# Kernel optimization log

Measured on AMD Instinct MI355X. Metric: run time of the kernel, lower is better.

Reference implementation:

```python
import jax, jax.numpy as jnp
import numpy as np

B, D, R, E, L = 8192, 2048, 64, 4, 3


def setup_inputs() -> dict:
    key = jax.random.key(0)
    ks = jax.random.split(key, 6)
    inputs = jax.random.normal(ks[0], (B, D), dtype=jnp.float32)
    # xavier-normal-ish init for low-rank factors
    U = jax.random.normal(ks[1], (L, E, D, R), dtype=jnp.float32) * (2.0 / (D + R)) ** 0.5
    V = jax.random.normal(ks[2], (L, E, D, R), dtype=jnp.float32) * (2.0 / (D + R)) ** 0.5
    C = jax.random.normal(ks[3], (L, E, R, R), dtype=jnp.float32) * (1.0 / R) ** 0.5
    gate_w = jax.random.normal(ks[4], (E, D), dtype=jnp.float32) * (1.0 / D) ** 0.5
    bias = jnp.zeros((L, D), dtype=jnp.float32)
    return {"inputs": inputs, "U": U, "V": V, "C": C, "gate_w": gate_w, "bias": bias}


def reference(inputs, U, V, C, gate_w, bias):
    x0 = inputs                      # (B, D)
    x_l = inputs
    for i in range(L):
        # gating scores per expert, softmax over experts
        gs = jax.nn.softmax(x_l @ gate_w.T, axis=-1)            # (B, E)
        # low-rank cross: tanh(V^T x) -> tanh(C .) -> U .
        vx = jnp.tanh(jnp.einsum('edr,bd->ber', V[i], x_l))     # (B, E, R)
        cx = jnp.tanh(jnp.einsum('esr,ber->bes', C[i], vx))     # (B, E, R)
        uv = jnp.einsum('eds,bes->bed', U[i], cx)               # (B, E, D)
        dot = (uv + bias[i][None, None, :]) * x0[:, None, :]    # (B, E, D)
        x_l = jnp.einsum('bed,be->bd', dot, gs) + x_l           # MoE combine + residual
    return x_l
```

## Files before the change

kernel.cpp:

```cpp
#include <hip/hip_runtime.h>
#include <cmath>

#define Bb 8192
#define Dd 2048
#define Rr 64
#define Ee 4
#define Ll 3

typedef __bf16 bf16x8 __attribute__((ext_vector_type(8)));
typedef float f32x4 __attribute__((ext_vector_type(4)));
typedef unsigned short u16x8 __attribute__((ext_vector_type(8)));
typedef unsigned short u16x4 __attribute__((ext_vector_type(4)));

__device__ __forceinline__ unsigned short f2bf(float f){
  unsigned u = __builtin_bit_cast(unsigned, f);
  u += 0x7fffu + ((u >> 16) & 1u);
  return (unsigned short)(u >> 16);
}
__device__ __forceinline__ float bf2f(unsigned short h){
  return __builtin_bit_cast(float, ((unsigned)h) << 16);
}

__global__ __launch_bounds__(256) void prep_w_k(const float* __restrict__ U,
                                                const float* __restrict__ V,
                                                const float* __restrict__ C,
                                                const float* __restrict__ gw,
                                                unsigned short* __restrict__ VfT,
                                                unsigned short* __restrict__ UfT,
                                                unsigned short* __restrict__ cb16,
                                                unsigned short* __restrict__ gw16){
  const int NV = Ll * 256 * Dd;
  const int NU = Ll * Dd * 256;
  const int NC = Ll * Ee * Rr * Rr;
  const int NG = Ee * Dd;
  const int total = NV + NU + NC + NG;
  for (int idx = blockIdx.x * blockDim.x + threadIdx.x; idx < total; idx += gridDim.x * blockDim.x){
    if (idx < NV){
      int l = idx / (256 * Dd); int rem = idx - l * 256 * Dd;
      int n = rem / Dd, d = rem - n * Dd;
      int e = n >> 6, r = n & 63;
      VfT[idx] = f2bf(V[(((size_t)l * Ee + e) * Dd + d) * Rr + r]);
    } else if (idx < NV + NU){
      int j = idx - NV;
      int l = j / (Dd * 256); int rem = j - l * Dd * 256;
      int d = rem / 256, k = rem - d * 256;
      int e = k >> 6, s = k & 63;
      UfT[j] = f2bf(U[(((size_t)l * Ee + e) * Dd + d) * Rr + s]);
    } else if (idx < NV + NU + NC){
      int j = idx - NV - NU;
      cb16[j] = f2bf(C[j]);
    } else {
      int j = idx - NV - NU - NC;
      gw16[j] = f2bf(gw[j]);
    }
  }
}

template<bool AF32>
__global__ __launch_bounds__(256) void gate_k(const void* __restrict__ xv,
                                              const unsigned short* __restrict__ gw16,
                                              float* __restrict__ gs){
  const int lane = threadIdx.x & 63;
  const int w = threadIdx.x >> 6;
  const int row = blockIdx.x * 4 + w;
  float s0 = 0.f, s1 = 0.f, s2 = 0.f, s3 = 0.f;
  #pragma unroll
  for (int c = 0; c < 4; c++){
    const int k = c * 512 + lane * 8;
    float xf[8];
    if constexpr (AF32){
      const float* xr = (const float*)xv + (size_t)row * Dd + k;
      f32x4 v0 = *(const f32x4*)xr;
      f32x4 v1 = *(const f32x4*)(xr + 4);
      #pragma unroll
      for (int u = 0; u < 4; u++){ xf[u] = v0[u]; xf[4 + u] = v1[u]; }
    } else {
      u16x8 xvv = *(const u16x8*)((const unsigned short*)xv + (size_t)row * Dd + k);
      #pragma unroll
      for (int u = 0; u < 8; u++) xf[u] = bf2f(xvv[u]);
    }
    u16x8 g0v = *(const u16x8*)(gw16 + 0 * Dd + k);
    u16x8 g1v = *(const u16x8*)(gw16 + 1 * Dd + k);
    u16x8 g2v = *(const u16x8*)(gw16 + 2 * Dd + k);
    u16x8 g3v = *(const u16x8*)(gw16 + 3 * Dd + k);
    #pragma unroll
    for (int u = 0; u < 8; u++){
      s0 += xf[u] * bf2f(g0v[u]);
      s1 += xf[u] * bf2f(g1v[u]);
      s2 += xf[u] * bf2f(g2v[u]);
      s3 += xf[u] * bf2f(g3v[u]);
    }
  }
  #pragma unroll
  for (int m = 1; m < 64; m <<= 1){
    s0 += __shfl_xor(s0, m, 64);
    s1 += __shfl_xor(s1, m, 64);
    s2 += __shfl_xor(s2, m, 64);
    s3 += __shfl_xor(s3, m, 64);
  }
  if (lane == 0){
    float mx = fmaxf(fmaxf(s0, s1), fmaxf(s2, s3));
    float e0 = __expf(s0 - mx), e1 = __expf(s1 - mx), e2 = __expf(s2 - mx), e3 = __expf(s3 - mx);
    float inv = 1.f / (e0 + e1 + e2 + e3);
    f32x4 g; g[0] = e0 * inv; g[1] = e1 * inv; g[2] = e2 * inv; g[3] = e3 * inv;
    *(f32x4*)(gs + (size_t)row * 4) = g;
  }
}

template<bool AF32>
__global__ __launch_bounds__(256) void gemm1_k(const void* __restrict__ Av,
                                               const unsigned short* __restrict__ BT,
                                               float* __restrict__ vxp){
  const int bm0 = blockIdx.x * 64;
  const int bn0 = blockIdx.y * 128;
  const int z   = blockIdx.z;
  const int kc0 = z * 512;
  const int tid = threadIdx.x;
  const int lane = tid & 63;
  const int wv = tid >> 6;
  const int wm = wv >> 1, wn = wv & 1;

  __shared__ __align__(16) char smraw[27648];
  unsigned short (*As)[72] = (unsigned short (*)[72])smraw;
  unsigned short (*Bs)[72] = (unsigned short (*)[72])(smraw + 9216);
  float (*epi)[132] = (float (*)[132])smraw;

  f32x4 acc[2][4] = {};
  const int arow = tid >> 2;
  const int aseg = tid & 3;

  const float* Af = (const float*)Av;
  const unsigned short* Ab = (const unsigned short*)Av;

  f32x4 a4[4]; u16x8 ar[2]; u16x8 br[4];
  if constexpr (AF32){
    #pragma unroll
    for (int j = 0; j < 4; j++)
      a4[j] = *(const f32x4*)(Af + (size_t)(bm0 + arow) * Dd + kc0 + aseg * 16 + j * 4);
  } else {
    ar[0] = *(const u16x8*)(Ab + (size_t)(bm0 + arow) * Dd + kc0 + aseg * 16);
    ar[1] = *(const u16x8*)(Ab + (size_t)(bm0 + arow) * Dd + kc0 + aseg * 16 + 8);
  }
  br[0] = *(const u16x8*)(BT + (size_t)(bn0 + arow) * Dd + kc0 + aseg * 16);
  br[1] = *(const u16x8*)(BT + (size_t)(bn0 + arow) * Dd + kc0 + aseg * 16 + 8);
  br[2] = *(const u16x8*)(BT + (size_t)(bn0 + arow + 64) * Dd + kc0 + aseg * 16);
  br[3] = *(const u16x8*)(BT + (size_t)(bn0 + arow + 64) * Dd + kc0 + aseg * 16 + 8);

  for (int k0 = kc0; k0 < kc0 + 512; k0 += 64){
    __syncthreads();
    if constexpr (AF32){
      u16x8 av0, av1;
      #pragma unroll
      for (int j = 0; j < 4; j++){
        av0[j] = f2bf(a4[0][j]); av0[4 + j] = f2bf(a4[1][j]);
        av1[j] = f2bf(a4[2][j]); av1[4 + j] = f2bf(a4[3][j]);
      }
      *(u16x8*)(&As[arow][aseg * 16])     = av0;
      *(u16x8*)(&As[arow][aseg * 16 + 8]) = av1;
    } else {
      *(u16x8*)(&As[arow][aseg * 16])     = ar[0];
      *(u16x8*)(&As[arow][aseg * 16 + 8]) = ar[1];
    }
    *(u16x8*)(&Bs[arow][aseg * 16])          = br[0];
    *(u16x8*)(&Bs[arow][aseg * 16 + 8])      = br[1];
    *(u16x8*)(&Bs[arow + 64][aseg * 16])     = br[2];
    *(u16x8*)(&Bs[arow + 64][aseg * 16 + 8]) = br[3];
    __syncthreads();

    int kn = k0 + 64;
    if (kn < kc0 + 512){
      if constexpr (AF32){
        #pragma unroll
        for (int j = 0; j < 4; j++)
          a4[j] = *(const f32x4*)(Af + (size_t)(bm0 + arow) * Dd + kn + aseg * 16 + j * 4);
      } else {
        ar[0] = *(const u16x8*)(Ab + (size_t)(bm0 + arow) * Dd + kn + aseg * 16);
        ar[1] = *(const u16x8*)(Ab + (size_t)(bm0 + arow) * Dd + kn + aseg * 16 + 8);
      }
      br[0] = *(const u16x8*)(BT + (size_t)(bn0 + arow) * Dd + kn + aseg * 16);
      br[1] = *(const u16x8*)(BT + (size_t)(bn0 + arow) * Dd + kn + aseg * 16 + 8);
      br[2] = *(const u16x8*)(BT + (size_t)(bn0 + arow + 64) * Dd + kn + aseg * 16);
      br[3] = *(const u16x8*)(BT + (size_t)(bn0 + arow + 64) * Dd + kn + aseg * 16 + 8);
    }

    #pragma unroll
    for (int ks = 0; ks < 2; ks++){
      bf16x8 af[2];
      #pragma unroll
      for (int mi = 0; mi < 2; mi++)
        af[mi] = *reinterpret_cast<const bf16x8*>(&As[wm * 32 + mi * 16 + (lane & 15)][ks * 32 + (lane >> 4) * 8]);
      #pragma unroll
      for (int nj = 0; nj < 4; nj++){
        bf16x8 bfr = *reinterpret_cast<const bf16x8*>(&Bs[wn * 64 + nj * 16 + (lane & 15)][ks * 32 + (lane >> 4) * 8]);
        #pragma unroll
        for (int mi = 0; mi < 2; mi++)
          acc[mi][nj] = __builtin_amdgcn_mfma_f32_16x16x32_bf16(af[mi], bfr, acc[mi][nj], 0, 0, 0);
      }
    }
  }

  float* outz = vxp + (size_t)z * Bb * 256;
  #pragma unroll
  for (int h = 0; h < 2; h++){
    __syncthreads();
    if (wm == h){
      #pragma unroll
      for (int mi = 0; mi < 2; mi++)
        #pragma unroll
        for (int nj = 0; nj < 4; nj++)
          #pragma unroll
          for (int q = 0; q < 4; q++)
            epi[mi * 16 + (lane >> 4) * 4 + q][wn * 64 + nj * 16 + (lane & 15)] = acc[mi][nj][q];
    }
    __syncthreads();
    #pragma unroll
    for (int c = 0; c < 4; c++){
      int idx = c * 256 + tid;
      int r = idx >> 5;
      int col = (idx & 31) * 4;
      *(f32x4*)(outz + (size_t)(bm0 + h * 32 + r) * 256 + bn0 + col) = *(const f32x4*)&epi[r][col];
    }
  }
}

__global__ __launch_bounds__(256) void gemm2_k(const float* __restrict__ vxp,
                                               const unsigned short* __restrict__ cb,
                                               const float* __restrict__ gs,
                                               unsigned short* __restrict__ wb){
  const int bm0 = blockIdx.x * 64;
  const int e   = blockIdx.y;
  const int tid = threadIdx.x;
  const int lane = tid & 63;
  const int wv = tid >> 6;
  const int wm = wv >> 1, wn = wv & 1;

  __shared__ __align__(16) char smraw[18432];
  unsigned short (*As)[72] = (unsigned short (*)[72])smraw;
  unsigned short (*Bs)[72] = (unsigned short (*)[72])(smraw + 9216);
  unsigned short (*epi)[72] = (unsigned short (*)[72])smraw;

  const int arow = tid >> 2;
  const int aseg = tid & 3;

  f32x4 t[4];
  #pragma unroll
  for (int j = 0; j < 4; j++)
    t[j] = *(const f32x4*)(vxp + (size_t)(bm0 + arow) * 256 + e * 64 + aseg * 16 + j * 4);
  #pragma unroll
  for (int z = 1; z < 4; z++)
    #pragma unroll
    for (int j = 0; j < 4; j++)
      t[j] += *(const f32x4*)(vxp + (size_t)z * Bb * 256 + (size_t)(bm0 + arow) * 256 + e * 64 + aseg * 16 + j * 4);
  u16x8 av0, av1;
  #pragma unroll
  for (int j = 0; j < 4; j++){
    av0[j] = f2bf(tanhf(t[0][j])); av0[4 + j] = f2bf(tanhf(t[1][j]));
    av1[j] = f2bf(tanhf(t[2][j])); av1[4 + j] = f2bf(tanhf(t[3][j]));
  }
  *(u16x8*)(&As[arow][aseg * 16]) = av0;
  *(u16x8*)(&As[arow][aseg * 16 + 8]) = av1;
  *(u16x8*)(&Bs[arow][aseg * 16])     = *(const u16x8*)(cb + e * 4096 + arow * 64 + aseg * 16);
  *(u16x8*)(&Bs[arow][aseg * 16 + 8]) = *(const u16x8*)(cb + e * 4096 + arow * 64 + aseg * 16 + 8);
  __syncthreads();

  f32x4 acc[2][2] = {};
  #pragma unroll
  for (int kk = 0; kk < 2; kk++){
    bf16x8 af[2];
    #pragma unroll
    for (int mi = 0; mi < 2; mi++)
      af[mi] = *reinterpret_cast<const bf16x8*>(&As[wm * 32 + mi * 16 + (lane & 15)][kk * 32 + (lane >> 4) * 8]);
    #pragma unroll
    for (int nj = 0; nj < 2; nj++){
      bf16x8 bfr = *reinterpret_cast<const bf16x8*>(&Bs[wn * 32 + nj * 16 + (lane & 15)][kk * 32 + (lane >> 4) * 8]);
      #pragma unroll
      for (int mi = 0; mi < 2; mi++)
        acc[mi][nj] = __builtin_amdgcn_mfma_f32_16x16x32_bf16(af[mi], bfr, acc[mi][nj], 0, 0, 0);
    }
  }

  __syncthreads();
  #pragma unroll
  for (int mi = 0; mi < 2; mi++)
    #pragma unroll
    for (int nj = 0; nj < 2; nj++)
      #pragma unroll
      for (int q = 0; q < 4; q++){
        int row = wm * 32 + mi * 16 + (lane >> 4) * 4 + q;
        int col = wn * 32 + nj * 16 + (lane & 15);
        float g = gs[(size_t)(bm0 + row) * 4 + e];
        epi[row][col] = f2bf(g * tanhf(acc[mi][nj][q]));
      }
  __syncthreads();
  #pragma unroll
  for (int c = 0; c < 2; c++){
    int idx = c * 256 + tid;
    int row = idx >> 3;
    int col = (idx & 7) * 8;
    *(u16x8*)(wb + (size_t)(bm0 + row) * 256 + e * 64 + col) = *(const u16x8*)(&epi[row][col]);
  }
}

template<int MODE>
__global__ __launch_bounds__(256, 4) void gemm3_k(const unsigned short* __restrict__ A,
                                                  const unsigned short* __restrict__ BT,
                                                  const float* __restrict__ x0f,
                                                  unsigned short* __restrict__ xst,
                                                  const float* __restrict__ biasrow,
                                                  float* __restrict__ out){
  const int bm0 = blockIdx.x * 64;
  const int bn0 = blockIdx.y * 128;
  const int tid = threadIdx.x;
  const int lane = tid & 63;
  const int wv = tid >> 6;
  const int wm = wv >> 1, wn = wv & 1;

  __shared__ __align__(16) char smraw[17408];
  unsigned short (*As)[40] = (unsigned short (*)[40])smraw;
  unsigned short (*Bs)[40] = (unsigned short (*)[40])(smraw + 5120);
  float (*epi)[132] = (float (*)[132])smraw;

  f32x4 acc[2][4] = {};
  const int arow = tid >> 2;
  const int aseg = tid & 3;

  f32x4 x0p[8];
  u16x4 xsp[8];
  #pragma unroll
  for (int h = 0; h < 2; h++)
    #pragma unroll
    for (int c = 0; c < 4; c++){
      int idx = c * 256 + tid;
      int r = idx >> 5;
      int col = (idx & 31) * 4;
      size_t o = (size_t)(bm0 + h * 32 + r) * Dd + bn0 + col;
      x0p[h * 4 + c] = *(const f32x4*)(x0f + o);
      if constexpr (MODE != 0) xsp[h * 4 + c] = *(const u16x4*)(xst + o);
    }

  u16x8 areg  = *(const u16x8*)(A  + (size_t)(bm0 + arow) * 256 + aseg * 8);
  u16x8 breg0 = *(const u16x8*)(BT + (size_t)(bn0 + arow) * 256 + aseg * 8);
  u16x8 breg1 = *(const u16x8*)(BT + (size_t)(bn0 + arow + 64) * 256 + aseg * 8);

  for (int k0 = 0; k0 < 256; k0 += 32){
    __syncthreads();
    *(u16x8*)(&As[arow][aseg * 8]) = areg;
    *(u16x8*)(&Bs[arow][aseg * 8]) = breg0;
    *(u16x8*)(&Bs[arow + 64][aseg * 8]) = breg1;
    __syncthreads();
    if (k0 + 32 < 256){
      areg  = *(const u16x8*)(A  + (size_t)(bm0 + arow) * 256 + k0 + 32 + aseg * 8);
      breg0 = *(const u16x8*)(BT + (size_t)(bn0 + arow) * 256 + k0 + 32 + aseg * 8);
      breg1 = *(const u16x8*)(BT + (size_t)(bn0 + arow + 64) * 256 + k0 + 32 + aseg * 8);
    }
    bf16x8 af[2];
    #pragma unroll
    for (int mi = 0; mi < 2; mi++)
      af[mi] = *reinterpret_cast<const bf16x8*>(&As[wm * 32 + mi * 16 + (lane & 15)][(lane >> 4) * 8]);
    #pragma unroll
    for (int nj = 0; nj < 4; nj++){
      bf16x8 bfr = *reinterpret_cast<const bf16x8*>(&Bs[wn * 64 + nj * 16 + (lane & 15)][(lane >> 4) * 8]);
      #pragma unroll
      for (int mi = 0; mi < 2; mi++)
        acc[mi][nj] = __builtin_amdgcn_mfma_f32_16x16x32_bf16(af[mi], bfr, acc[mi][nj], 0, 0, 0);
    }
  }

  #pragma unroll
  for (int h = 0; h < 2; h++){
    __syncthreads();
    if (wm == h){
      #pragma unroll
      for (int mi = 0; mi < 2; mi++)
        #pragma unroll
        for (int nj = 0; nj < 4; nj++)
          #pragma unroll
          for (int q = 0; q < 4; q++)
            epi[mi * 16 + (lane >> 4) * 4 + q][wn * 64 + nj * 16 + (lane & 15)] = acc[mi][nj][q];
    }
    __syncthreads();
    #pragma unroll
    for (int c = 0; c < 4; c++){
      int idx = c * 256 + tid;
      int r = idx >> 5;
      int col = (idx & 31) * 4;
      int row = bm0 + h * 32 + r;
      size_t o = (size_t)row * Dd + bn0 + col;
      f32x4 y = *(const f32x4*)&epi[r][col];
      f32x4 x0v = x0p[h * 4 + c];
      f32x4 bv  = *(const f32x4*)(biasrow + bn0 + col);
      f32x4 xo;
      if constexpr (MODE == 0){
        xo = x0v;
      } else {
        u16x4 xv = xsp[h * 4 + c];
        #pragma unroll
        for (int j = 0; j < 4; j++) xo[j] = bf2f(xv[j]);
      }
      f32x4 xn;
      #pragma unroll
      for (int j = 0; j < 4; j++) xn[j] = xo[j] + x0v[j] * (bv[j] + y[j]);
      if constexpr (MODE == 2){
        *(f32x4*)(out + o) = xn;
      } else {
        u16x4 xnb;
        #pragma unroll
        for (int j = 0; j < 4; j++) xnb[j] = f2bf(xn[j]);
        *(u16x4*)(xst + o) = xnb;
      }
    }
  }
}

extern "C" void kernel_launch(void* const* d_in, const int* in_sizes, int n_in,
                              void* d_out, int out_size, void* d_ws, size_t ws_size,
                              hipStream_t stream){
  (void)in_sizes; (void)n_in; (void)out_size;
  const float* inp  = (const float*)d_in[0];
  const float* U    = (const float*)d_in[1];
  const float* V    = (const float*)d_in[2];
  const float* C    = (const float*)d_in[3];
  const float* gw   = (const float*)d_in[4];
  const float* bias = (const float*)d_in[5];
  float* out = (float*)d_out;

  char* ws = (char*)d_ws;
  size_t o = 0;
  unsigned short* xb  = (unsigned short*)(ws + o); o += (size_t)Bb * Dd * 2;
  float*          vxp = (float*)(ws + o);          o += (size_t)4 * Bb * 256 * 4;
  unsigned short* wb  = (unsigned short*)(ws + o); o += (size_t)Bb * 256 * 2;
  float*          gsb = (float*)(ws + o);          o += (size_t)Bb * 4 * 4;
  unsigned short* vft = (unsigned short*)(ws + o); o += (size_t)Ll * 256 * Dd * 2;
  unsigned short* uft = (unsigned short*)(ws + o); o += (size_t)Ll * Dd * 256 * 2;
  unsigned short* cb16= (unsigned short*)(ws + o); o += (size_t)Ll * Ee * Rr * Rr * 2;
  unsigned short* g16 = (unsigned short*)(ws + o); o += (size_t)Ee * Dd * 2;
  if (ws_size < o) return;

  prep_w_k<<<1024, 256, 0, stream>>>(U, V, C, gw, vft, uft, cb16, g16);

  for (int l = 0; l < Ll; l++){
    if (l == 0){
      gate_k<true><<<Bb / 4, 256, 0, stream>>>(inp, g16, gsb);
      gemm1_k<true><<<dim3(Bb / 64, 2, 4), 256, 0, stream>>>(inp, vft + (size_t)l * 256 * Dd, vxp);
    } else {
      gate_k<false><<<Bb / 4, 256, 0, stream>>>(xb, g16, gsb);
      gemm1_k<false><<<dim3(Bb / 64, 2, 4), 256, 0, stream>>>(xb, vft + (size_t)l * 256 * Dd, vxp);
    }
    gemm2_k<<<dim3(Bb / 64, Ee), 256, 0, stream>>>(vxp, cb16 + (size_t)l * Ee * Rr * Rr, gsb, wb);
    const unsigned short* uftl = uft + (size_t)l * Dd * 256;
    if (l == 0)
      gemm3_k<0><<<dim3(Bb / 64, Dd / 128), 256, 0, stream>>>(wb, uftl, inp, xb, bias + (size_t)l * Dd, out);
    else if (l == 1)
      gemm3_k<1><<<dim3(Bb / 64, Dd / 128), 256, 0, stream>>>(wb, uftl, inp, xb, bias + (size_t)l * Dd, out);
    else
      gemm3_k<2><<<dim3(Bb / 64, Dd / 128), 256, 0, stream>>>(wb, uftl, inp, xb, bias + (size_t)l * Dd, out);
  }
}
```

Measured before the change: 248.2 us.

## Fuse gating logits into gemm3 epilogue, store split-K partials and x0 as bf16

Gate logits for the next layer are now computed in the gemm3 epilogue as per-column-tile partial dot products and reduced with softmax inside gemm2. This removes the separate gate kernel, which re-read the full activation matrix for layers 1 and 2. The split-K partials from gemm1 are stored as bf16 instead of fp32, halving that round trip. A bf16 copy of the input is made once and used as x0 in every gemm3 epilogue, and the x0 and x_l prefetch before the main loop is dropped. The costs are extra bf16 rounding of the partial sums and x0, plus an extra cast kernel.

Result: faster. 218.0 us (-12.2%).

```diff
diff --git a/kernel.cpp b/kernel.cpp
--- a/kernel.cpp
+++ b/kernel.cpp
@@ -19,6 +19,17 @@
 }
 __device__ __forceinline__ float bf2f(unsigned short h){
   return __builtin_bit_cast(float, ((unsigned)h) << 16);
+}
+
+__global__ __launch_bounds__(256) void cast_x_k(const float* __restrict__ x,
+                                                unsigned short* __restrict__ xb0){
+  const int n4 = Bb * Dd / 4;
+  for (int i = blockIdx.x * blockDim.x + threadIdx.x; i < n4; i += gridDim.x * blockDim.x){
+    f32x4 v = *((const f32x4*)x + i);
+    u16x4 o;
+    o[0] = f2bf(v[0]); o[1] = f2bf(v[1]); o[2] = f2bf(v[2]); o[3] = f2bf(v[3]);
+    *((u16x4*)xb0 + i) = o;
+  }
 }
 
 __global__ __launch_bounds__(256) void prep_w_k(const float* __restrict__ U,
@@ -110,7 +121,7 @@
 template<bool AF32>
 __global__ __launch_bounds__(256) void gemm1_k(const void* __restrict__ Av,
                                                const unsigned short* __restrict__ BT,
-                                               float* __restrict__ vxp){
+                                               unsigned short* __restrict__ vxp){
   const int bm0 = blockIdx.x * 64;
   const int bn0 = blockIdx.y * 128;
   const int z   = blockIdx.z;
@@ -199,7 +210,7 @@
     }
   }
 
-  float* outz = vxp + (size_t)z * Bb * 256;
+  unsigned short* outz = vxp + (size_t)z * Bb * 256;
   #pragma unroll
   for (int h = 0; h < 2; h++){
     __syncthreads();
@@ -218,14 +229,20 @@
       int idx = c * 256 + tid;
       int r = idx >> 5;
       int col = (idx & 31) * 4;
-      *(f32x4*)(outz + (size_t)(bm0 + h * 32 + r) * 256 + bn0 + col) = *(const f32x4*)&epi[r][col];
-    }
-  }
-}
-
-__global__ __launch_bounds__(256) void gemm2_k(const float* __restrict__ vxp,
+      f32x4 v = *(const f32x4*)&epi[r][col];
+      u16x4 ov;
+      #pragma unroll
+      for (int j = 0; j < 4; j++) ov[j] = f2bf(v[j]);
+      *(u16x4*)(outz + (size_t)(bm0 + h * 32 + r) * 256 + bn0 + col) = ov;
+    }
+  }
+}
+
+template<bool FROMPLOG>
+__global__ __launch_bounds__(256) void gemm2_k(const unsigned short* __restrict__ vxp,
                                                const unsigned short* __restrict__ cb,
-                                               const float* __restrict__ gs,
+                                               const float* __restrict__ gsb,
+                                               const float* __restrict__ plog,
                                                unsigned short* __restrict__ wb){
   const int bm0 = blockIdx.x * 64;
   const int e   = blockIdx.y;
@@ -234,28 +251,53 @@
   const int wv = tid >> 6;
   const int wm = wv >> 1, wn = wv & 1;
 
-  __shared__ __align__(16) char smraw[18432];
+  __shared__ __align__(16) char smraw[19456];
   unsigned short (*As)[72] = (unsigned short (*)[72])smraw;
   unsigned short (*Bs)[72] = (unsigned short (*)[72])(smraw + 9216);
+  float (*gs_l)[4] = (float (*)[4])(smraw + 18432);
   unsigned short (*epi)[72] = (unsigned short (*)[72])smraw;
+
+  if constexpr (FROMPLOG){
+    int r = tid >> 2, q = tid & 3;
+    f32x4 s = {0.f, 0.f, 0.f, 0.f};
+    #pragma unroll
+    for (int ci = 0; ci < 4; ci++)
+      s += *(const f32x4*)(plog + ((size_t)(q * 4 + ci) * Bb + bm0 + r) * 4);
+    #pragma unroll
+    for (int j = 0; j < 4; j++){
+      s[j] += __shfl_xor(s[j], 1, 64);
+      s[j] += __shfl_xor(s[j], 2, 64);
+    }
+    if (q == 0){
+      float mx = fmaxf(fmaxf(s[0], s[1]), fmaxf(s[2], s[3]));
+      float e0 = __expf(s[0] - mx), e1 = __expf(s[1] - mx), e2 = __expf(s[2] - mx), e3 = __expf(s[3] - mx);
+      float inv = 1.f / (e0 + e1 + e2 + e3);
+      f32x4 g; g[0] = e0 * inv; g[1] = e1 * inv; g[2] = e2 * inv; g[3] = e3 * inv;
+      *(f32x4*)&gs_l[r][0] = g;
+    }
+  } else {
+    if (tid < 64) *(f32x4*)&gs_l[tid][0] = *(const f32x4*)(gsb + (size_t)(bm0 + tid) * 4);
+  }
 
   const int arow = tid >> 2;
   const int aseg = tid & 3;
 
-  f32x4 t[4];
-  #pragma unroll
-  for (int j = 0; j < 4; j++)
-    t[j] = *(const f32x4*)(vxp + (size_t)(bm0 + arow) * 256 + e * 64 + aseg * 16 + j * 4);
-  #pragma unroll
-  for (int z = 1; z < 4; z++)
-    #pragma unroll
-    for (int j = 0; j < 4; j++)
-      t[j] += *(const f32x4*)(vxp + (size_t)z * Bb * 256 + (size_t)(bm0 + arow) * 256 + e * 64 + aseg * 16 + j * 4);
+  float tv[16];
+  #pragma unroll
+  for (int j = 0; j < 16; j++) tv[j] = 0.f;
+  #pragma unroll
+  for (int z = 0; z < 4; z++){
+    const unsigned short* vz = vxp + ((size_t)z * Bb + bm0 + arow) * 256 + e * 64 + aseg * 16;
+    u16x8 p0 = *(const u16x8*)vz;
+    u16x8 p1 = *(const u16x8*)(vz + 8);
+    #pragma unroll
+    for (int j = 0; j < 8; j++){ tv[j] += bf2f(p0[j]); tv[8 + j] += bf2f(p1[j]); }
+  }
   u16x8 av0, av1;
   #pragma unroll
   for (int j = 0; j < 4; j++){
-    av0[j] = f2bf(tanhf(t[0][j])); av0[4 + j] = f2bf(tanhf(t[1][j]));
-    av1[j] = f2bf(tanhf(t[2][j])); av1[4 + j] = f2bf(tanhf(t[3][j]));
+    av0[j] = f2bf(tanhf(tv[j]));     av0[4 + j] = f2bf(tanhf(tv[4 + j]));
+    av1[j] = f2bf(tanhf(tv[8 + j])); av1[4 + j] = f2bf(tanhf(tv[12 + j]));
   }
   *(u16x8*)(&As[arow][aseg * 16]) = av0;
   *(u16x8*)(&As[arow][aseg * 16 + 8]) = av1;
@@ -288,7 +330,7 @@
       for (int q = 0; q < 4; q++){
         int row = wm * 32 + mi * 16 + (lane >> 4) * 4 + q;
         int col = wn * 32 + nj * 16 + (lane & 15);
-        float g = gs[(size_t)(bm0 + row) * 4 + e];
+        float g = gs_l[row][e];
         epi[row][col] = f2bf(g * tanhf(acc[mi][nj][q]));
       }
   __syncthreads();
@@ -301,13 +343,16 @@
   }
 }
 
-template<int MODE>
+template<int MODE, bool X0BF>
 __global__ __launch_bounds__(256, 4) void gemm3_k(const unsigned short* __restrict__ A,
                                                   const unsigned short* __restrict__ BT,
                                                   const float* __restrict__ x0f,
+                                                  const unsigned short* __restrict__ x0b,
                                                   unsigned short* __restrict__ xst,
                                                   const float* __restrict__ biasrow,
-                                                  float* __restrict__ out){
+                                                  float* __restrict__ out,
+                                                  const unsigned short* __restrict__ gw16,
+                                                  float* __restrict__ plog){
   const int bm0 = blockIdx.x * 64;
   const int bn0 = blockIdx.y * 128;
   const int tid = threadIdx.x;
@@ -323,20 +368,6 @@
   f32x4 acc[2][4] = {};
   const int arow = tid >> 2;
   const int aseg = tid & 3;
-
-  f32x4 x0p[8];
-  u16x4 xsp[8];
-  #pragma unroll
-  for (int h = 0; h < 2; h++)
-    #pragma unroll
-    for (int c = 0; c < 4; c++){
-      int idx = c * 256 + tid;
-      int r = idx >> 5;
-      int col = (idx & 31) * 4;
-      size_t o = (size_t)(bm0 + h * 32 + r) * Dd + bn0 + col;
-      x0p[h * 4 + c] = *(const f32x4*)(x0f + o);
-      if constexpr (MODE != 0) xsp[h * 4 + c] = *(const u16x4*)(xst + o);
-    }
 
   u16x8 areg  = *(const u16x8*)(A  + (size_t)(bm0 + arow) * 256 + aseg * 8);
   u16x8 breg0 = *(const u16x8*)(BT + (size_t)(bn0 + arow) * 256 + aseg * 8);
@@ -387,13 +418,20 @@
       int row = bm0 + h * 32 + r;
       size_t o = (size_t)row * Dd + bn0 + col;
       f32x4 y = *(const f32x4*)&epi[r][col];
-      f32x4 x0v = x0p[h * 4 + c];
-      f32x4 bv  = *(const f32x4*)(biasrow + bn0 + col);
+      f32x4 bv = *(const f32x4*)(biasrow + bn0 + col);
+      f32x4 x0v;
+      if constexpr (X0BF){
+        u16x4 xv = *(const u16x4*)(x0b + o);
+        #pragma unroll
+        for (int j = 0; j < 4; j++) x0v[j] = bf2f(xv[j]);
+      } else {
+        x0v = *(const f32x4*)(x0f + o);
+      }
       f32x4 xo;
       if constexpr (MODE == 0){
         xo = x0v;
       } else {
-        u16x4 xv = xsp[h * 4 + c];
+        u16x4 xv = *(const u16x4*)(xst + o);
         #pragma unroll
         for (int j = 0; j < 4; j++) xo[j] = bf2f(xv[j]);
       }
@@ -407,6 +445,23 @@
         #pragma unroll
         for (int j = 0; j < 4; j++) xnb[j] = f2bf(xn[j]);
         *(u16x4*)(xst + o) = xnb;
+      }
+      if constexpr (MODE != 2){
+        float s[4];
+        #pragma unroll
+        for (int e = 0; e < 4; e++){
+          u16x4 gv = *(const u16x4*)(gw16 + (size_t)e * Dd + bn0 + col);
+          s[e] = xn[0] * bf2f(gv[0]) + xn[1] * bf2f(gv[1])
+               + xn[2] * bf2f(gv[2]) + xn[3] * bf2f(gv[3]);
+        }
+        #pragma unroll
+        for (int m = 1; m < 32; m <<= 1)
+          #pragma unroll
+          for (int e = 0; e < 4; e++) s[e] += __shfl_xor(s[e], m, 64);
+        if ((tid & 31) == 0){
+          f32x4 pv; pv[0] = s[0]; pv[1] = s[1]; pv[2] = s[2]; pv[3] = s[3];
+          *(f32x4*)(plog + ((size_t)blockIdx.y * Bb + row) * 4) = pv;
+        }
       }
     }
   }
@@ -427,32 +482,54 @@
   char* ws = (char*)d_ws;
   size_t o = 0;
   unsigned short* xb  = (unsigned short*)(ws + o); o += (size_t)Bb * Dd * 2;
-  float*          vxp = (float*)(ws + o);          o += (size_t)4 * Bb * 256 * 4;
+  unsigned short* vxp = (unsigned short*)(ws + o); o += (size_t)4 * Bb * 256 * 2;
   unsigned short* wb  = (unsigned short*)(ws + o); o += (size_t)Bb * 256 * 2;
   float*          gsb = (float*)(ws + o);          o += (size_t)Bb * 4 * 4;
+  float*          plog= (float*)(ws + o);          o += (size_t)16 * Bb * 4 * 4;
   unsigned short* vft = (unsigned short*)(ws + o); o += (size_t)Ll * 256 * Dd * 2;
   unsigned short* uft = (unsigned short*)(ws + o); o += (size_t)Ll * Dd * 256 * 2;
   unsigned short* cb16= (unsigned short*)(ws + o); o += (size_t)Ll * Ee * Rr * Rr * 2;
   unsigned short* g16 = (unsigned short*)(ws + o); o += (size_t)Ee * Dd * 2;
   if (ws_size < o) return;
+  unsigned short* x0b = nullptr;
+  if (ws_size >= o + (size_t)Bb * Dd * 2){
+    x0b = (unsigned short*)(ws + o); o += (size_t)Bb * Dd * 2;
+  }
+  const bool hx = (x0b != nullptr);
 
   prep_w_k<<<1024, 256, 0, stream>>>(U, V, C, gw, vft, uft, cb16, g16);
+  if (hx) cast_x_k<<<2048, 256, 0, stream>>>(inp, x0b);
 
   for (int l = 0; l < Ll; l++){
+    const unsigned short* vftl = vft + (size_t)l * 256 * Dd;
+    const unsigned short* uftl = uft + (size_t)l * Dd * 256;
+    const unsigned short* cbl  = cb16 + (size_t)l * Ee * Rr * Rr;
+    const float* biasl = bias + (size_t)l * Dd;
+
     if (l == 0){
-      gate_k<true><<<Bb / 4, 256, 0, stream>>>(inp, g16, gsb);
-      gemm1_k<true><<<dim3(Bb / 64, 2, 4), 256, 0, stream>>>(inp, vft + (size_t)l * 256 * Dd, vxp);
+      if (hx){
+        gate_k<false><<<Bb / 4, 256, 0, stream>>>(x0b, g16, gsb);
+        gemm1_k<false><<<dim3(Bb / 64, 2, 4), 256, 0, stream>>>(x0b, vftl, vxp);
+      } else {
+        gate_k<true><<<Bb / 4, 256, 0, stream>>>(inp, g16, gsb);
+        gemm1_k<true><<<dim3(Bb / 64, 2, 4), 256, 0, stream>>>(inp, vftl, vxp);
+      }
+      gemm2_k<false><<<dim3(Bb / 64, Ee), 256, 0, stream>>>(vxp, cbl, gsb, plog, wb);
     } else {
-      gate_k<false><<<Bb / 4, 256, 0, stream>>>(xb, g16, gsb);
-      gemm1_k<false><<<dim3(Bb / 64, 2, 4), 256, 0, stream>>>(xb, vft + (size_t)l * 256 * Dd, vxp);
-    }
-    gemm2_k<<<dim3(Bb / 64, Ee), 256, 0, stream>>>(vxp, cb16 + (size_t)l * Ee * Rr * Rr, gsb, wb);
-    const unsigned short* uftl = uft + (size_t)l * Dd * 256;
-    if (l == 0)
-      gemm3_k<0><<<dim3(Bb / 64, Dd / 128), 256, 0, stream>>>(wb, uftl, inp, xb, bias + (size_t)l * Dd, out);
-    else if (l == 1)
-      gemm3_k<1><<<dim3(Bb / 64, Dd / 128), 256, 0, stream>>>(wb, uftl, inp, xb, bias + (size_t)l * Dd, out);
-    else
-      gemm3_k<2><<<dim3(Bb / 64, Dd / 128), 256, 0, stream>>>(wb, uftl, inp, xb, bias + (size_t)l * Dd, out);
-  }
-}
+      gemm1_k<false><<<dim3(Bb / 64, 2, 4), 256, 0, stream>>>(xb, vftl, vxp);
+      gemm2_k<true><<<dim3(Bb / 64, Ee), 256, 0, stream>>>(vxp, cbl, gsb, plog, wb);
+    }
+
+    dim3 g3(Bb / 64, Dd / 128);
+    if (l == 0){
+      if (hx) gemm3_k<0, true ><<<g3, 256, 0, stream>>>(wb, uftl, inp, x0b, xb, biasl, out, g16, plog);
+      else    gemm3_k<0, false><<<g3, 256, 0, stream>>>(wb, uftl, inp, x0b, xb, biasl, out, g16, plog);
+    } else if (l == 1){
+      if (hx) gemm3_k<1, true ><<<g3, 256, 0, stream>>>(wb, uftl, inp, x0b, xb, biasl, out, g16, plog);
+      else    gemm3_k<1, false><<<g3, 256, 0, stream>>>(wb, uftl, inp, x0b, xb, biasl, out, g16, plog);
+    } else {
+      if (hx) gemm3_k<2, true ><<<g3, 256, 0, stream>>>(wb, uftl, inp, x0b, xb, biasl, out, g16, plog);
+      else    gemm3_k<2, false><<<g3, 256, 0, stream>>>(wb, uftl, inp, x0b, xb, biasl, out, g16, plog);
+    }
+  }
+}
```
